# Performance work log

Hardware: AMD Instinct MI355X
Metric: run time of the kernel (lower is better)

The kernel has to match this reference:

```python
import jax, jax.numpy as jnp
import numpy as np

EPS = 1e-08


def setup_inputs() -> dict:
    key = jax.random.key(0)
    k1, = jax.random.split(key, 1)
    B, T, F = 64, 1000, 257
    mag = jax.random.uniform(k1, (B, T, F), dtype=jnp.float32)
    s = jnp.zeros((B, F), dtype=jnp.float32)
    weights = jnp.ones((1, 1, F), dtype=jnp.float32)
    bias = jnp.zeros((1, 1, F), dtype=jnp.float32)
    alpha = jnp.full((1, F), -4.0, dtype=jnp.float32)
    return {"mag": mag, "s": s, "weights": weights, "bias": bias, "alpha": alpha}


def reference(mag, s, weights, bias, alpha):
    # mag: [B, T, F]; s: [B, F] initial EMA state
    power = mag * mag                      # [B, T, F]
    a = jax.nn.sigmoid(alpha)              # [1, F], broadcasts over B

    def step(carry, p_t):
        # carry: [B, F], p_t: [B, F]
        new = carry * (1.0 - a) + p_t * a
        return new, new

    # scan over time axis: move T to leading axis
    _, smooth = jax.lax.scan(step, s, jnp.swapaxes(power, 0, 1))  # smooth: [T, B, F]
    smooth_data = jnp.sqrt(jnp.swapaxes(smooth, 0, 1))            # [B, T, F]
    return mag / (smooth_data + EPS) * weights + bias
```

## Files before the change

kernel.cpp:

```cpp
#include <hip/hip_runtime.h>

#define EPS 1e-8f


template <int L>
__global__ __launch_bounds__(256)
void fns4_aggregate(const float* __restrict__ mag,
                    const float* __restrict__ alpha,
                    float* __restrict__ S,
                    int B, int T, int F, int C) {
    const int BF = B * F;
    int g = blockIdx.x * blockDim.x + threadIdx.x;
    if (g >= BF * C) return;
    const int bf = g % BF;
    const int c  = g / BF;
    const int b  = bf / F;
    const int f  = bf - b * F;

    const float a   = 1.0f / (1.0f + expf(-alpha[f]));
    const float oma = 1.0f - a;

    const float* p = mag + ((size_t)b * T + (size_t)c * L) * F + f;

    float local = 0.0f;
#pragma unroll
    for (int t = 0; t < L; ++t) {
        float m = p[(size_t)t * F];
        local = local * oma + (m * m) * a;
    }
    S[(size_t)c * BF + bf] = local;
}

template <int L>
__global__ __launch_bounds__(256)
void fns4_emit(const float* __restrict__ mag,
               const float* __restrict__ s0,
               const float* __restrict__ weights,
               const float* __restrict__ bias,
               const float* __restrict__ alpha,
               const float* __restrict__ S,
               float* __restrict__ out,
               int B, int T, int F, int C) {
    const int BF = B * F;
    int g = blockIdx.x * blockDim.x + threadIdx.x;
    if (g >= BF * C) return;
    const int bf = g % BF;
    const int c  = g / BF;
    const int b  = bf / F;
    const int f  = bf - b * F;

    const float a   = 1.0f / (1.0f + expf(-alpha[f]));
    const float oma = 1.0f - a;
    const float w   = weights[f];
    const float bi  = bias[f];

    float carry = s0[bf];
    if (c > 0) {
        const float D = powf(oma, (float)L);
        for (int j = 0; j < c; ++j)
            carry = carry * D + S[(size_t)j * BF + bf];
    }

    const float* p = mag + ((size_t)b * T + (size_t)c * L) * F + f;
    float*       o = out + ((size_t)b * T + (size_t)c * L) * F + f;

#pragma unroll
    for (int t = 0; t < L; ++t) {
        float m = p[(size_t)t * F];
        carry = carry * oma + (m * m) * a;
        o[(size_t)t * F] = m / (sqrtf(carry) + EPS) * w + bi;
    }
}

__global__ void fns4_fallback(const float* __restrict__ mag,
                              const float* __restrict__ s0,
                              const float* __restrict__ weights,
                              const float* __restrict__ bias,
                              const float* __restrict__ alpha,
                              float* __restrict__ out,
                              int B, int T, int F) {
    int bf = blockIdx.x * blockDim.x + threadIdx.x;
    int BF = B * F;
    if (bf >= BF) return;
    int b = bf / F;
    int f = bf - b * F;

    float a  = 1.0f / (1.0f + expf(-alpha[f]));
    float w  = weights[f];
    float bi = bias[f];

    float carry = s0[bf];
    const float* p = mag + (size_t)b * T * F + f;
    float*       o = out + (size_t)b * T * F + f;

    for (int t = 0; t < T; ++t) {
        float m = p[(size_t)t * F];
        carry = carry * (1.0f - a) + (m * m) * a;
        o[(size_t)t * F] = m / (sqrtf(carry) + EPS) * w + bi;
    }
}

extern "C" void kernel_launch(void* const* d_in, const int* in_sizes, int n_in,
                              void* d_out, int out_size, void* d_ws, size_t ws_size,
                              hipStream_t stream) {
    const float* mag     = (const float*)d_in[0];
    const float* s0      = (const float*)d_in[1];
    const float* weights = (const float*)d_in[2];
    const float* bias    = (const float*)d_in[3];
    const float* alpha   = (const float*)d_in[4];
    float* out = (float*)d_out;

    int F  = in_sizes[4];
    int BF = in_sizes[1];
    int B  = BF / F;
    int T  = in_sizes[0] / BF;

    constexpr int L = 50;
    if (T % L == 0) {
        int C = T / L;
        size_t need = (size_t)C * BF * sizeof(float);
        if (ws_size >= need) {
            float* S = (float*)d_ws;
            int total  = BF * C;
            int blocks = (total + 255) / 256;
            fns4_aggregate<L><<<blocks, 256, 0, stream>>>(
                mag, alpha, S, B, T, F, C);
            fns4_emit<L><<<blocks, 256, 0, stream>>>(
                mag, s0, weights, bias, alpha, S, out, B, T, F, C);
            return;
        }
    }

    int threads = 256;
    int blocks  = (BF + threads - 1) / threads;
    fns4_fallback<<<blocks, threads, 0, stream>>>(mag, s0, weights, bias,
                                                  alpha, out, B, T, F);
}
```

Measured before the change: 46.64 us.

## Fuse aggregate and emit passes into one cooperative kernel with grid sync

Merges the chunk-aggregate and emit kernels into a single cooperative kernel. A grid-wide sync separates computing per-chunk EMA partial sums from the carry-propagation and output pass. This removes one kernel launch and its gap. It requires every block (about 1285 of 256 threads) to be resident at once, and if the cooperative launch is rejected the code falls back to the two-kernel path. It also replaces powf for the chunk decay with an unrolled multiply loop.

```diff
diff --git a/kernel.cpp b/kernel.cpp
--- a/kernel.cpp
+++ b/kernel.cpp
@@ -1,7 +1,65 @@
 #include <hip/hip_runtime.h>
+#include <hip/hip_cooperative_groups.h>
+
+namespace cg = cooperative_groups;
 
 #define EPS 1e-8f
 
+template <int L>
+__global__ __launch_bounds__(256, 6)
+void fns5_fused(const float* __restrict__ mag,
+                const float* __restrict__ s0,
+                const float* __restrict__ weights,
+                const float* __restrict__ bias,
+                const float* __restrict__ alpha,
+                float* __restrict__ out,
+                float* __restrict__ S,
+                int B, int T, int F, int C) {
+    const int BF = B * F;
+    const int g  = blockIdx.x * blockDim.x + threadIdx.x;
+    const bool valid = g < BF * C;
+    const int bf = valid ? g % BF : 0;
+    const int c  = valid ? g / BF : 0;
+    const int b  = bf / F;
+    const int f  = bf - b * F;
+
+    const float a   = 1.0f / (1.0f + expf(-alpha[f]));
+    const float oma = 1.0f - a;
+
+    const float* p = mag + ((size_t)b * T + (size_t)c * L) * F + f;
+
+    float local = 0.0f;
+#pragma unroll
+    for (int t = 0; t < L; ++t) {
+        float m = valid ? p[(size_t)t * F] : 0.0f;
+        local = local * oma + (m * m) * a;
+    }
+    if (valid)
+        S[(size_t)c * BF + bf] = local;
+
+    cg::this_grid().sync();
+
+    float carry = valid ? s0[bf] : 0.0f;
+    if (c > 0) {
+        float D = 1.0f;
+#pragma unroll
+        for (int i = 0; i < L; ++i) D *= oma;
+        for (int j = 0; j < c; ++j)
+            carry = carry * D + S[(size_t)j * BF + bf];
+    }
+
+    const float w  = weights[f];
+    const float bi = bias[f];
+    float* o = out + ((size_t)b * T + (size_t)c * L) * F + f;
+
+#pragma unroll
+    for (int t = 0; t < L; ++t) {
+        float m = valid ? p[(size_t)t * F] : 0.0f;
+        carry = carry * oma + (m * m) * a;
+        float r = m / (sqrtf(carry) + EPS) * w + bi;
+        if (valid) o[(size_t)t * F] = r;
+    }
+}
 
 template <int L>
 __global__ __launch_bounds__(256)
@@ -19,7 +77,6 @@
 
     const float a   = 1.0f / (1.0f + expf(-alpha[f]));
     const float oma = 1.0f - a;
-
     const float* p = mag + ((size_t)b * T + (size_t)c * L) * F + f;
 
     float local = 0.0f;
@@ -56,7 +113,9 @@
 
     float carry = s0[bf];
     if (c > 0) {
-        const float D = powf(oma, (float)L);
+        float D = 1.0f;
+#pragma unroll
+        for (int i = 0; i < L; ++i) D *= oma;
         for (int j = 0; j < c; ++j)
             carry = carry * D + S[(size_t)j * BF + bf];
     }
@@ -72,13 +131,13 @@
     }
 }
 
-__global__ void fns4_fallback(const float* __restrict__ mag,
-                              const float* __restrict__ s0,
-                              const float* __restrict__ weights,
-                              const float* __restrict__ bias,
-                              const float* __restrict__ alpha,
-                              float* __restrict__ out,
-                              int B, int T, int F) {
+__global__ void fns_fallback(const float* __restrict__ mag,
+                             const float* __restrict__ s0,
+                             const float* __restrict__ weights,
+                             const float* __restrict__ bias,
+                             const float* __restrict__ alpha,
+                             float* __restrict__ out,
+                             int B, int T, int F) {
     int bf = blockIdx.x * blockDim.x + threadIdx.x;
     int BF = B * F;
     if (bf >= BF) return;
@@ -123,6 +182,16 @@
             float* S = (float*)d_ws;
             int total  = BF * C;
             int blocks = (total + 255) / 256;
+
+            void* args[] = {(void*)&mag, (void*)&s0, (void*)&weights,
+                            (void*)&bias, (void*)&alpha, (void*)&out,
+                            (void*)&S, (void*)&B, (void*)&T, (void*)&F,
+                            (void*)&C};
+            hipError_t e = hipLaunchCooperativeKernel(
+                (void*)fns5_fused<L>, dim3(blocks), dim3(256),
+                args, 0, stream);
+            if (e == hipSuccess) return;
+
             fns4_aggregate<L><<<blocks, 256, 0, stream>>>(
                 mag, alpha, S, B, T, F, C);
             fns4_emit<L><<<blocks, 256, 0, stream>>>(
@@ -133,6 +202,6 @@
 
     int threads = 256;
     int blocks  = (BF + threads - 1) / threads;
-    fns4_fallback<<<blocks, threads, 0, stream>>>(mag, s0, weights, bias,
-                                                  alpha, out, B, T, F);
-}
+    fns_fallback<<<blocks, threads, 0, stream>>>(mag, s0, weights, bias,
+                                                 alpha, out, B, T, F);
+}
```

Result: slower. 183.8 us (+294.2%).

## Split scan into aggregate, prefix, and emit kernels with smaller chunks

Applied to the files above, without the earlier changes.

Replaces the two-kernel chunked scan with three kernels. Chunks shrink from 50 to 25 steps, which doubles thread-level parallelism. A separate prefix kernel computes each chunk's starting carry once, so the emit kernel no longer repeats an O(c) serial loop over chunk summaries per thread. Loads are batched in groups of 5 behind a compiler barrier so several memory reads are in flight at once, and the division becomes a hardware reciprocal. The cost is an extra kernel launch and a workspace write and read of the prefix array, and the reciprocal is slightly less precise.

```diff
diff --git a/kernel.cpp b/kernel.cpp
--- a/kernel.cpp
+++ b/kernel.cpp
@@ -2,6 +2,119 @@
 
 #define EPS 1e-8f
 
+__device__ __forceinline__ float sigmoidf_(float x) {
+    return 1.0f / (1.0f + expf(-x));
+}
+
+
+template <int LS, int BT>
+__global__ __launch_bounds__(256)
+void fns9_aggregate(const float* __restrict__ mag,
+                    const float* __restrict__ alpha,
+                    float* __restrict__ S,
+                    int B, int T, int F, int Cs1) {
+    static_assert(LS % BT == 0, "");
+    const int BF = B * F;
+    int g = blockIdx.x * blockDim.x + threadIdx.x;
+    if (g >= BF * Cs1) return;
+    const int bf = g % BF;
+    const int j  = g / BF;
+    const int b  = bf / F;
+    const int f  = bf - b * F;
+
+    const float a   = sigmoidf_(alpha[f]);
+    const float oma = 1.0f - a;
+
+    const float* p = mag + ((size_t)b * T + (size_t)j * LS) * F + f;
+
+    float local = 0.0f;
+#pragma unroll
+    for (int blk = 0; blk < LS / BT; ++blk) {
+        float m[BT];
+#pragma unroll
+        for (int i = 0; i < BT; ++i)
+            m[i] = p[(size_t)(blk * BT + i) * F];
+        asm volatile("" ::: "memory");
+#pragma unroll
+        for (int i = 0; i < BT; ++i)
+            local = local * oma + (m[i] * m[i]) * a;
+    }
+    S[(size_t)j * BF + bf] = local;
+}
+
+template <int LS>
+__global__ __launch_bounds__(256)
+void fns9_prefix(const float* __restrict__ s0,
+                 const float* __restrict__ alpha,
+                 const float* __restrict__ S,
+                 float* __restrict__ P,
+                 int B, int F, int Cs) {
+    const int BF = B * F;
+    int bf = blockIdx.x * blockDim.x + threadIdx.x;
+    if (bf >= BF) return;
+    const int b = bf / F;
+    const int f = bf - b * F;
+
+    const float a   = sigmoidf_(alpha[f]);
+    const float oma = 1.0f - a;
+    float D = 1.0f;
+#pragma unroll
+    for (int i = 0; i < LS; ++i) D *= oma;
+
+    float carry = s0[bf];
+    for (int j = 0; j < Cs; ++j) {
+        P[(size_t)j * BF + bf] = carry;
+        if (j < Cs - 1)
+            carry = carry * D + S[(size_t)j * BF + bf];
+    }
+}
+
+template <int LS, int BT>
+__global__ __launch_bounds__(256)
+void fns9_emit(const float* __restrict__ mag,
+               const float* __restrict__ weights,
+               const float* __restrict__ bias,
+               const float* __restrict__ alpha,
+               const float* __restrict__ P,
+               float* __restrict__ out,
+               int B, int T, int F, int Cs) {
+    static_assert(LS % BT == 0, "");
+    const int BF = B * F;
+    int g = blockIdx.x * blockDim.x + threadIdx.x;
+    if (g >= BF * Cs) return;
+    const int bf = g % BF;
+    const int j  = g / BF;
+    const int b  = bf / F;
+    const int f  = bf - b * F;
+
+    const float a   = sigmoidf_(alpha[f]);
+    const float oma = 1.0f - a;
+    const float w   = weights[f];
+    const float bi  = bias[f];
+
+    float carry = P[(size_t)j * BF + bf];
+
+    const float* p = mag + ((size_t)b * T + (size_t)j * LS) * F + f;
+    float*       o = out + ((size_t)b * T + (size_t)j * LS) * F + f;
+
+#pragma unroll
+    for (int blk = 0; blk < LS / BT; ++blk) {
+        float m[BT];
+#pragma unroll
+        for (int i = 0; i < BT; ++i)
+            m[i] = p[(size_t)(blk * BT + i) * F];
+        asm volatile("" ::: "memory");
+        float r[BT];
+#pragma unroll
+        for (int i = 0; i < BT; ++i) {
+            carry = carry * oma + (m[i] * m[i]) * a;
+            r[i] = m[i] * __builtin_amdgcn_rcpf(sqrtf(carry) + EPS) * w + bi;
+        }
+#pragma unroll
+        for (int i = 0; i < BT; ++i)
+            o[(size_t)(blk * BT + i) * F] = r[i];
+    }
+}
 
 template <int L>
 __global__ __launch_bounds__(256)
@@ -17,9 +130,8 @@
     const int b  = bf / F;
     const int f  = bf - b * F;
 
-    const float a   = 1.0f / (1.0f + expf(-alpha[f]));
-    const float oma = 1.0f - a;
-
+    const float a   = sigmoidf_(alpha[f]);
+    const float oma = 1.0f - a;
     const float* p = mag + ((size_t)b * T + (size_t)c * L) * F + f;
 
     float local = 0.0f;
@@ -49,14 +161,16 @@
     const int b  = bf / F;
     const int f  = bf - b * F;
 
-    const float a   = 1.0f / (1.0f + expf(-alpha[f]));
+    const float a   = sigmoidf_(alpha[f]);
     const float oma = 1.0f - a;
     const float w   = weights[f];
     const float bi  = bias[f];
 
     float carry = s0[bf];
     if (c > 0) {
-        const float D = powf(oma, (float)L);
+        float D = 1.0f;
+#pragma unroll
+        for (int i = 0; i < L; ++i) D *= oma;
         for (int j = 0; j < c; ++j)
             carry = carry * D + S[(size_t)j * BF + bf];
     }
@@ -72,20 +186,20 @@
     }
 }
 
-__global__ void fns4_fallback(const float* __restrict__ mag,
-                              const float* __restrict__ s0,
-                              const float* __restrict__ weights,
-                              const float* __restrict__ bias,
-                              const float* __restrict__ alpha,
-                              float* __restrict__ out,
-                              int B, int T, int F) {
+__global__ void fns_fallback(const float* __restrict__ mag,
+                             const float* __restrict__ s0,
+                             const float* __restrict__ weights,
+                             const float* __restrict__ bias,
+                             const float* __restrict__ alpha,
+                             float* __restrict__ out,
+                             int B, int T, int F) {
     int bf = blockIdx.x * blockDim.x + threadIdx.x;
     int BF = B * F;
     if (bf >= BF) return;
     int b = bf / F;
     int f = bf - b * F;
 
-    float a  = 1.0f / (1.0f + expf(-alpha[f]));
+    float a  = sigmoidf_(alpha[f]);
     float w  = weights[f];
     float bi = bias[f];
 
@@ -115,17 +229,40 @@
     int B  = BF / F;
     int T  = in_sizes[0] / BF;
 
+    constexpr int LS = 25;
+    constexpr int BT = 5;
+    if (T % LS == 0) {
+        int Cs  = T / LS;
+        int Cs1 = Cs - 1;
+        size_t sBytes = (size_t)Cs1 * BF * sizeof(float);
+        size_t pOff   = (sBytes + 255) & ~(size_t)255;
+        size_t need   = pOff + (size_t)Cs * BF * sizeof(float);
+        if (Cs1 >= 1 && ws_size >= need) {
+            float* S = (float*)d_ws;
+            float* P = (float*)((char*)d_ws + pOff);
+
+            int n1 = BF * Cs1;
+            int n3 = BF * Cs;
+            fns9_aggregate<LS, BT><<<(n1 + 255) / 256, 256, 0, stream>>>(
+                mag, alpha, S, B, T, F, Cs1);
+            fns9_prefix<LS><<<(BF + 255) / 256, 256, 0, stream>>>(
+                s0, alpha, S, P, B, F, Cs);
+            fns9_emit<LS, BT><<<(n3 + 255) / 256, 256, 0, stream>>>(
+                mag, weights, bias, alpha, P, out, B, T, F, Cs);
+            return;
+        }
+    }
+
     constexpr int L = 50;
     if (T % L == 0) {
         int C = T / L;
         size_t need = (size_t)C * BF * sizeof(float);
         if (ws_size >= need) {
             float* S = (float*)d_ws;
-            int total  = BF * C;
-            int blocks = (total + 255) / 256;
-            fns4_aggregate<L><<<blocks, 256, 0, stream>>>(
+            int n = BF * C;
+            fns4_aggregate<L><<<(n + 255) / 256, 256, 0, stream>>>(
                 mag, alpha, S, B, T, F, C);
-            fns4_emit<L><<<blocks, 256, 0, stream>>>(
+            fns4_emit<L><<<(n + 255) / 256, 256, 0, stream>>>(
                 mag, s0, weights, bias, alpha, S, out, B, T, F, C);
             return;
         }
@@ -133,6 +270,6 @@
 
     int threads = 256;
     int blocks  = (BF + threads - 1) / threads;
-    fns4_fallback<<<blocks, threads, 0, stream>>>(mag, s0, weights, bias,
-                                                  alpha, out, B, T, F);
-}
+    fns_fallback<<<blocks, threads, 0, stream>>>(mag, s0, weights, bias,
+                                                 alpha, out, B, T, F);
+}
```

New measurement: 56.25 us. 1.21x slower.
